# Kernel tuning notes

Hardware: AMD Instinct MI355X
Metric: run time of the kernel (lower is better)

The kernel has to match this reference:

```python
import jax, jax.numpy as jnp
import numpy as np

NUM_RELATIONS = 8
NUM_BASES = 4
IN_CH, HID, OUT_CH = 128, 64, 64
N_NODES, N_EDGES = 50000, 500000


def rgcn_conv(x, edge_src, edge_dst, edge_type, basis, comp, root, bias):
    """PyG RGCNConv with basis decomposition and per-relation mean aggregation.
    basis: [B, in, out], comp: [R, B], root: [in, out], bias: [out].
    W_r = sum_b comp[r, b] * basis[b]; msg_e = x[src_e] @ W_{type_e};
    aggregate mean over incoming edges per (node, relation), sum over relations,
    then add root transform and bias.
    """
    n = x.shape[0]
    out_dim = basis.shape[2]
    # Project once through all bases: [N, B, out]  (cheap: B=4)
    h = jnp.einsum('ni,bio->nbo', x, basis)
    # Per-edge message: contract gathered basis features with per-edge comp coeffs
    msg = jnp.einsum('eb,ebo->eo', comp[edge_type], h[edge_src])  # [E, out]
    # Mean aggregation per (dst, relation): segment id = dst*R + relation
    seg = edge_dst * NUM_RELATIONS + edge_type
    sums = jax.ops.segment_sum(msg, seg, num_segments=n * NUM_RELATIONS)
    cnt = jax.ops.segment_sum(jnp.ones((msg.shape[0], 1), msg.dtype), seg,
                              num_segments=n * NUM_RELATIONS)
    mean = sums / jnp.maximum(cnt, 1.0)
    agg = mean.reshape(n, NUM_RELATIONS, out_dim).sum(axis=1)
    return agg + x @ root + bias


def setup_inputs() -> dict:
    key = jax.random.key(0)
    ks = jax.random.split(key, 12)
    s1 = 1.0 / np.sqrt(IN_CH)
    s2 = 1.0 / np.sqrt(HID)
    return {
        'x': jax.random.normal(ks[0], (N_NODES, IN_CH), jnp.float32),
        'edge_index': jax.random.randint(ks[1], (2, N_EDGES), 0, N_NODES, jnp.int64),
        'edge_type': jax.random.randint(ks[2], (N_EDGES,), 0, NUM_RELATIONS, jnp.int64),
        'basis1': jax.random.normal(ks[3], (NUM_BASES, IN_CH, HID), jnp.float32) * s1,
        'comp1': jax.random.normal(ks[4], (NUM_RELATIONS, NUM_BASES), jnp.float32) * 0.5,
        'root1': jax.random.normal(ks[5], (IN_CH, HID), jnp.float32) * s1,
        'bias1': jnp.zeros((HID,), jnp.float32),
        'basis2': jax.random.normal(ks[6], (NUM_BASES, HID, OUT_CH), jnp.float32) * s2,
        'comp2': jax.random.normal(ks[7], (NUM_RELATIONS, NUM_BASES), jnp.float32) * 0.5,
        'root2': jax.random.normal(ks[8], (HID, OUT_CH), jnp.float32) * s2,
        'bias2': jnp.zeros((OUT_CH,), jnp.float32),
    }


def reference(x, edge_index, edge_type, basis1, comp1, root1, bias1,
              basis2, comp2, root2, bias2):
    src, dst = edge_index[0], edge_index[1]
    h = rgcn_conv(x, src, dst, edge_type, basis1, comp1, root1, bias1)
    h = jax.nn.relu(h)
    out = rgcn_conv(h, src, dst, edge_type, basis2, comp2, root2, bias2)
    return out
```

## Files before the change

kernel.cpp:

```cpp
#include <hip/hip_runtime.h>
#include <cstddef>

#define NREL 8
#define SCAN_TILE 4096

typedef __bf16 bf16x8 __attribute__((ext_vector_type(8)));
typedef float f32x4 __attribute__((ext_vector_type(4)));
typedef unsigned short ushort_t;

__device__ __forceinline__ unsigned f2bf_u(float f) {
    unsigned u = __float_as_uint(f);
    u += 0x7FFFu + ((u >> 16) & 1u);
    return u >> 16;
}
__device__ __forceinline__ short f2bf(float f) { return (short)f2bf_u(f); }
__device__ __forceinline__ int pack2bf(float lo, float hi) {
    return (int)(f2bf_u(lo) | (f2bf_u(hi) << 16));
}
__device__ __forceinline__ float bfval(unsigned short g) {
    return __uint_as_float((unsigned)g << 16);
}

__global__ __launch_bounds__(256) void zero_kernel(int4* __restrict__ p, int n16,
                                                   int* __restrict__ offsN, int E)
{
    int i = blockIdx.x * 256 + threadIdx.x;
    if (i < n16) p[i] = make_int4(0, 0, 0, 0);
    if (i == 0) *offsN = E;
}

template<int K>
__device__ __forceinline__ void wfrag_body(const float* __restrict__ basis,
                                           const float* __restrict__ root,
                                           const float* __restrict__ comp,
                                           short* __restrict__ Wf, int tid)
{
    constexpr int NK = K / 32;
    int lane = tid & 63, slot = tid >> 6;
    int ks = slot % NK, t = slot / NK;
    int kg = lane >> 4, lr = lane & 15;
    int k0 = ks * 32 + kg * 8;
    union { short s[8]; int4 v; } u;
#pragma unroll
    for (int e = 0; e < 8; ++e) {
        int k = k0 + e;
        float v;
        if (t < 32) {
            int rr = t >> 2, ch = (t & 3) * 16 + lr;
            v = comp[rr * 4 + 0] * basis[((size_t)0 * K + k) * 64 + ch]
              + comp[rr * 4 + 1] * basis[((size_t)1 * K + k) * 64 + ch]
              + comp[rr * 4 + 2] * basis[((size_t)2 * K + k) * 64 + ch]
              + comp[rr * 4 + 3] * basis[((size_t)3 * K + k) * 64 + ch];
        } else {
            v = root[(size_t)k * 64 + (t - 32) * 16 + lr];
        }
        u.s[e] = f2bf(v);
    }
    *(int4*)(Wf + (size_t)tid * 8) = u.v;
}

__device__ __forceinline__ void afrag_body128(const float* __restrict__ x,
                                              short* __restrict__ xf, int N, int tid)
{
    int lane = tid & 63, slot = tid >> 6;
    int ks = slot & 3, rt = slot >> 2;
    int kg = lane >> 4, lr = lane & 15;
    int row = rt * 16 + lr, k = ks * 32 + kg * 8;
    union { short s[8]; int4 v; } u;
    if (row < N) {
        const float* xp = x + (size_t)row * 128 + k;
        float4 a = *(const float4*)xp;
        float4 b = *(const float4*)(xp + 4);
        u.s[0] = f2bf(a.x); u.s[1] = f2bf(a.y); u.s[2] = f2bf(a.z); u.s[3] = f2bf(a.w);
        u.s[4] = f2bf(b.x); u.s[5] = f2bf(b.y); u.s[6] = f2bf(b.z); u.s[7] = f2bf(b.w);
    } else {
        u.v = make_int4(0, 0, 0, 0);
    }
    *(int4*)(xf + (size_t)tid * 8) = u.v;
}

__global__ __launch_bounds__(256) void prep_hist_kernel(
    const int* __restrict__ dstp, const int* __restrict__ et, int* __restrict__ cnt8,
    const float* __restrict__ basis1, const float* __restrict__ root1,
    const float* __restrict__ comp1,  const float* __restrict__ basis2,
    const float* __restrict__ root2,  const float* __restrict__ comp2,
    const float* __restrict__ x,
    short* __restrict__ Wf1, short* __restrict__ Wf2, short* __restrict__ xf1,
    int E, int N, int NT, int HB)
{
    int b = blockIdx.x;
    if (b < HB) {
        int e = b * 256 + threadIdx.x;
        if (e < E) atomicAdd(&cnt8[dstp[e] * NREL + et[e]], 1);
        return;
    }
    b -= HB;
    if (b < 36) { wfrag_body<128>(basis1, root1, comp1, Wf1, b * 256 + threadIdx.x); return; }
    b -= 36;
    if (b < 18) { wfrag_body<64>(basis2, root2, comp2, Wf2, b * 256 + threadIdx.x); return; }
    b -= 18;
    int tid = b * 256 + threadIdx.x;
    if (tid < NT * 256) afrag_body128(x, xf1, N, tid);
}

__global__ __launch_bounds__(256) void scan_part(const int* __restrict__ cnt8,
                                                 int* __restrict__ tsum, int n)
{
    int base = blockIdx.x * SCAN_TILE;
    int s = 0;
    for (int i = threadIdx.x; i < SCAN_TILE; i += 256) {
        int idx = base + i;
        if (idx < n) {
            int4 a = ((const int4*)cnt8)[idx * 2];
            int4 b = ((const int4*)cnt8)[idx * 2 + 1];
            s += a.x + a.y + a.z + a.w + b.x + b.y + b.z + b.w;
        }
    }
    for (int d = 1; d < 64; d <<= 1) s += __shfl_xor(s, d, 64);
    __shared__ int ws[4];
    if ((threadIdx.x & 63) == 0) ws[threadIdx.x >> 6] = s;
    __syncthreads();
    if (threadIdx.x == 0) tsum[blockIdx.x] = ws[0] + ws[1] + ws[2] + ws[3];
}

__global__ __launch_bounds__(256) void scan_final(const int* __restrict__ cnt8,
                                                  const int* __restrict__ tsum,
                                                  int* __restrict__ offs, int n)
{
    const int lane = threadIdx.x & 63, wid = threadIdx.x >> 6;
    int tbase = 0;
    for (int i = 0; i < blockIdx.x; ++i) tbase += tsum[i];
    int base = blockIdx.x * SCAN_TILE + threadIdx.x * 16;
    int v[16]; int s = 0;
#pragma unroll
    for (int j = 0; j < 16; ++j) {
        int idx = base + j;
        int dv = 0;
        if (idx < n) {
            int4 a = ((const int4*)cnt8)[idx * 2];
            int4 b = ((const int4*)cnt8)[idx * 2 + 1];
            dv = a.x + a.y + a.z + a.w + b.x + b.y + b.z + b.w;
        }
        v[j] = dv; s += dv;
    }
    int inc = s;
    for (int d = 1; d < 64; d <<= 1) {
        int t = __shfl_up(inc, d, 64);
        if (lane >= d) inc += t;
    }
    __shared__ int wsum[4];
    if (lane == 63) wsum[wid] = inc;
    __syncthreads();
    int run = tbase + (inc - s);
    for (int k = 0; k < wid; ++k) run += wsum[k];
#pragma unroll
    for (int j = 0; j < 16; ++j) {
        int idx = base + j;
        if (idx < n) offs[idx] = run;
        run += v[j];
    }
}

__global__ __launch_bounds__(256) void scatter_kernel(const int* __restrict__ src,
                                                      const int* __restrict__ dst,
                                                      const int* __restrict__ et,
                                                      const int* __restrict__ offs,
                                                      int* __restrict__ cursor,
                                                      const int* __restrict__ cnt8,
                                                      int4* __restrict__ edgeP, int E)
{
    int e = blockIdx.x * 256 + threadIdx.x;
    if (e >= E) return;
    int d = dst[e], r = et[e], s = src[e];
    int c = cnt8[d * NREL + r];
    float inv = 1.0f / (float)(c > 1 ? c : 1);
    int pos = offs[d] + atomicAdd(&cursor[d], 1);
    edgeP[pos] = make_int4((s * NREL + r) * 64, __float_as_int(inv), d, 0);
}

template<int K, bool L2OUT>
__global__ __launch_bounds__(256) void gemm_mfma(const short* __restrict__ xf,
                                                 const short* __restrict__ Wf,
                                                 const float* __restrict__ bias,
                                                 short* __restrict__ hr,
                                                 float* __restrict__ rootF,
                                                 int N, int gblk)
{
    constexpr int NK = K / 32;
    __shared__ short lds[4 * NK * 512];

    const int w = threadIdx.x >> 6, lane = threadIdx.x & 63;
    const int kg = lane >> 4, lr = lane & 15;
    const int g = blockIdx.y;

    {
        const int4* gsrc = (const int4*)(Wf + (size_t)g * 4 * NK * 512);
        int4* ldst = (int4*)lds;
        for (int i = threadIdx.x; i < 4 * NK * 64; i += 256)
            ldst[i] = gsrc[i];
    }

    float b0 = bias[lr], b1 = bias[16 + lr], b2 = bias[32 + lr], b3 = bias[48 + lr];

    __syncthreads();

    for (int bx = blockIdx.x; bx < gblk; bx += gridDim.x) {
        const int rt = bx * 4 + w;

        bf16x8 afrag[NK];
        const short* ap = xf + ((size_t)rt * NK * 64 + lane) * 8;
#pragma unroll
        for (int ks = 0; ks < NK; ++ks)
            afrag[ks] = *(const bf16x8*)(ap + ks * 512);

        f32x4 acc[4];
#pragma unroll
        for (int t = 0; t < 4; ++t) acc[t] = (f32x4){0.f, 0.f, 0.f, 0.f};

#pragma unroll
        for (int tt = 0; tt < 4; ++tt) {
#pragma unroll
            for (int ks = 0; ks < NK; ++ks) {
                bf16x8 bfrag = *(const bf16x8*)(lds + (tt * NK + ks) * 512 + lane * 8);
                acc[tt] = __builtin_amdgcn_mfma_f32_16x16x32_bf16(afrag[ks], bfrag,
                                                                  acc[tt], 0, 0, 0);
            }
        }

        const int drow0 = rt * 16 + kg * 4;
#pragma unroll
        for (int r = 0; r < 4; ++r) {
            int dr = drow0 + r;
            if (dr >= N) break;
            if (g < 8) {
                int u0 = pack2bf(acc[0][r], acc[1][r]);
                int u1 = pack2bf(acc[2][r], acc[3][r]);
                *(int2*)(hr + (size_t)dr * 512 + g * 64 + lr * 4) = make_int2(u0, u1);
            } else if (!L2OUT) {
                f32x4 o = {acc[0][r] + b0, acc[1][r] + b1, acc[2][r] + b2, acc[3][r] + b3};
                *(f32x4*)(rootF + (size_t)dr * 64 + lr * 4) = o;
            } else {
                rootF[(size_t)dr * 64 + lr]      = acc[0][r] + b0;
                rootF[(size_t)dr * 64 + 16 + lr] = acc[1][r] + b1;
                rootF[(size_t)dr * 64 + 32 + lr] = acc[2][r] + b2;
                rootF[(size_t)dr * 64 + 48 + lr] = acc[3][r] + b3;
            }
        }
    }
}

template<bool PERM>
__global__ __launch_bounds__(256) void agg_chunk_kernel(
    const int4* __restrict__ edgeP, const short* __restrict__ hr,
    float* __restrict__ accF, int E)
{
    const int w = threadIdx.x >> 6, l = threadIdx.x & 63;
    const int base = (blockIdx.x * 4 + w) * 32;
    if (base >= E) return;
    const int nv = min(32, E - base);

    int idx = base + (l & 31);
    if (idx >= E) idx = E - 1;
    int4 pl = edgeP[idx];

    const unsigned short* hp = (const unsigned short*)hr;

    int g[32];
#pragma unroll
    for (int j = 0; j < 32; ++j) {
        int hoff = __shfl(pl.x, j);
        g[j] = hp[(size_t)hoff + l];
    }

    const int co = PERM ? ((l & 3) * 16 + (l >> 2)) : l;

    float acc = 0.f;
#pragma unroll
    for (int j = 0; j < 32; ++j) {
        if (j >= nv) break;
        float invj = __uint_as_float(__shfl(pl.y, j));
        acc = fmaf(bfval((unsigned short)g[j]), invj, acc);
        int dcur = __shfl(pl.z, j);
        int dnxt = __shfl(pl.z, (j + 1) & 31);
        if (j == nv - 1 || dnxt != dcur) {
            unsafeAtomicAdd(&accF[(size_t)dcur * 64 + co], acc);
            acc = 0.f;
        }
    }
}

__global__ __launch_bounds__(256) void fin1_kernel(const float* __restrict__ aggF,
                                                   short* __restrict__ outB, int N)
{
    int i = blockIdx.x * 256 + threadIdx.x;
    if (i >= N * 64) return;
    int dst = i >> 6, l = i & 63;
    float v = fmaxf(aggF[i], 0.f);
    int tc = (l & 3) * 16 + (l >> 2);
    int rt2 = dst >> 4, lr2 = dst & 15;
    int ks2 = tc >> 5, kg2 = (tc >> 3) & 3, e2 = tc & 7;
    outB[(((size_t)rt2 * 2 + ks2) * 64 + kg2 * 16 + lr2) * 8 + e2] = f2bf(v);
}

extern "C" void kernel_launch(void* const* d_in, const int* in_sizes, int n_in,
                              void* d_out, int out_size, void* d_ws, size_t ws_size,
                              hipStream_t stream)
{
    const float* x      = (const float*)d_in[0];
    const int*   ei     = (const int*)d_in[1];
    const int*   et     = (const int*)d_in[2];
    const float* basis1 = (const float*)d_in[3];
    const float* comp1  = (const float*)d_in[4];
    const float* root1  = (const float*)d_in[5];
    const float* bias1  = (const float*)d_in[6];
    const float* basis2 = (const float*)d_in[7];
    const float* comp2  = (const float*)d_in[8];
    const float* root2  = (const float*)d_in[9];
    const float* bias2  = (const float*)d_in[10];
    float* out = (float*)d_out;

    const int N = in_sizes[0] / 128;
    const int E = in_sizes[2];
    const int* src  = ei;
    const int* dstp = ei + E;

    const int gblk = (N + 63) / 64;
    const int NT   = gblk * 4;
    const int HB   = (E + 255) / 256;

    char* p = (char*)d_ws;
    auto carve = [&](size_t bytes) -> char* {
        char* q = p; p += (bytes + 255) & ~(size_t)255; return q;
    };
    int*   cursor  = (int*)carve((size_t)N * 4);
    int*   cnt8    = (int*)carve((size_t)N * NREL * 4);
    char*  zend    = p;
    float* aggF1   = (float*)carve((size_t)N * 64 * 4);
    int*   offs    = (int*)carve((size_t)(N + 1) * 4);
    int*   tsum    = (int*)carve(256 * 4);
    int4*  edgeP   = (int4*)carve((size_t)E * 16);
    short* Wf1     = (short*)carve((size_t)36 * 4 * 64 * 8 * 2);
    short* Wf2     = (short*)carve((size_t)36 * 2 * 64 * 8 * 2);
    short* xf1     = (short*)carve((size_t)NT * 4 * 64 * 8 * 2);
    short* xf2     = (short*)carve((size_t)NT * 2 * 64 * 8 * 2);
    short* hr      = (short*)carve((size_t)N * 512 * 2);

    const int zn16 = (int)((zend - (char*)cursor) / 16);
    const int ntiles = (N + SCAN_TILE - 1) / SCAN_TILE;
    const int CHB = (E + 127) / 128;
    const int FB  = (N * 64 + 255) / 256;

    zero_kernel<<<(zn16 + 255) / 256, 256, 0, stream>>>((int4*)cursor, zn16, offs + N, E);

    prep_hist_kernel<<<HB + 36 + 18 + NT, 256, 0, stream>>>(
        dstp, et, cnt8, basis1, root1, comp1, basis2, root2, comp2, x,
        Wf1, Wf2, xf1, E, N, NT, HB);

    scan_part<<<ntiles, 256, 0, stream>>>(cnt8, tsum, N);
    scan_final<<<ntiles, 256, 0, stream>>>(cnt8, tsum, offs, N);

    scatter_kernel<<<HB, 256, 0, stream>>>(src, dstp, et, offs, cursor,
                                           cnt8, edgeP, E);

    gemm_mfma<128, false><<<dim3(256, 9), 256, 0, stream>>>(xf1, Wf1, bias1, hr,
                                                            aggF1, N, gblk);
    agg_chunk_kernel<false><<<CHB, 256, 0, stream>>>(edgeP, hr, aggF1, E);
    fin1_kernel<<<FB, 256, 0, stream>>>(aggF1, xf2, N);

    gemm_mfma<64, true><<<dim3(256, 9), 256, 0, stream>>>(xf2, Wf2, bias2, hr,
                                                          out, N, gblk);
    agg_chunk_kernel<true><<<CHB, 256, 0, stream>>>(edgeP, hr, out, E);
}
```

Measured before the change: 165.4 us.

## Process two edges per wavefront with 32-bit paired-channel gathers in aggregation

The aggregation kernel now gives each wavefront 64 edges, with half-waves handling even and odd edges. Each lane loads a 32-bit word holding two bf16 channels instead of one 16-bit value, and issues two atomics per flush. This halves the number of gather instructions and block launches, at the cost of twice as many atomics per lane and more complex validity and flush logic. The GEMM grid x-dimension also changes from a fixed 256 to half the block-group count, which alters how work is spread across blocks.

```diff
diff --git a/kernel.cpp b/kernel.cpp
--- a/kernel.cpp
+++ b/kernel.cpp
@@ -175,7 +175,7 @@
     int c = cnt8[d * NREL + r];
     float inv = 1.0f / (float)(c > 1 ? c : 1);
     int pos = offs[d] + atomicAdd(&cursor[d], 1);
-    edgeP[pos] = make_int4((s * NREL + r) * 64, __float_as_int(inv), d, 0);
+    edgeP[pos] = make_int4((s * NREL + r) * 32, __float_as_int(inv), d, 0);
 }
 
 template<int K, bool L2OUT>
@@ -255,36 +255,51 @@
     float* __restrict__ accF, int E)
 {
     const int w = threadIdx.x >> 6, l = threadIdx.x & 63;
-    const int base = (blockIdx.x * 4 + w) * 32;
+    const int half = l >> 5, c = l & 31;
+    const int base = (blockIdx.x * 4 + w) * 64;
     if (base >= E) return;
-    const int nv = min(32, E - base);
-
-    int idx = base + (l & 31);
+    const int nv = min(64, E - base);
+
+    int idx = base + 2 * c + half;
     if (idx >= E) idx = E - 1;
     int4 pl = edgeP[idx];
 
-    const unsigned short* hp = (const unsigned short*)hr;
-
-    int g[32];
+    const unsigned* hp32 = (const unsigned*)hr;
+
+    unsigned g[32];
 #pragma unroll
     for (int j = 0; j < 32; ++j) {
-        int hoff = __shfl(pl.x, j);
-        g[j] = hp[(size_t)hoff + l];
-    }
-
-    const int co = PERM ? ((l & 3) * 16 + (l >> 2)) : l;
-
-    float acc = 0.f;
+        int he = __shfl(pl.x, j);
+        int ho = __shfl(pl.x, 32 + j);
+        int hoff = half ? ho : he;
+        g[j] = hp32[(size_t)hoff + c];
+    }
+
+    int out0, out1;
+    if (PERM) {
+        int s0 = 2 * c, s1 = 2 * c + 1;
+        out0 = (s0 & 3) * 16 + (s0 >> 2);
+        out1 = (s1 & 3) * 16 + (s1 >> 2);
+    } else {
+        out0 = 2 * c; out1 = 2 * c + 1;
+    }
+
+    float a0 = 0.f, a1 = 0.f;
 #pragma unroll
     for (int j = 0; j < 32; ++j) {
-        if (j >= nv) break;
-        float invj = __uint_as_float(__shfl(pl.y, j));
-        acc = fmaf(bfval((unsigned short)g[j]), invj, acc);
-        int dcur = __shfl(pl.z, j);
-        int dnxt = __shfl(pl.z, (j + 1) & 31);
-        if (j == nv - 1 || dnxt != dcur) {
-            unsafeAtomicAdd(&accF[(size_t)dcur * 64 + co], acc);
-            acc = 0.f;
+        int jj = 2 * j + half;
+        bool valid = jj < nv;
+        float invj = __uint_as_float(__shfl(pl.y, half * 32 + j));
+        float v0 = bfval((unsigned short)(g[j] & 0xFFFFu));
+        float v1 = bfval((unsigned short)(g[j] >> 16));
+        if (valid) { a0 = fmaf(v0, invj, a0); a1 = fmaf(v1, invj, a1); }
+        int dcur = __shfl(pl.z, half * 32 + j);
+        int dnxt = (j < 31) ? __shfl(pl.z, half * 32 + j + 1) : -1;
+        bool flush = valid && (j == 31 || jj + 2 >= nv || dnxt != dcur);
+        if (flush) {
+            unsafeAtomicAdd(&accF[(size_t)dcur * 64 + out0], a0);
+            unsafeAtomicAdd(&accF[(size_t)dcur * 64 + out1], a1);
+            a0 = 0.f; a1 = 0.f;
         }
     }
 }
@@ -327,6 +342,7 @@
     const int gblk = (N + 63) / 64;
     const int NT   = gblk * 4;
     const int HB   = (E + 255) / 256;
+    const int GX   = (gblk + 1) / 2;
 
     char* p = (char*)d_ws;
     auto carve = [&](size_t bytes) -> char* {
@@ -347,7 +363,7 @@
 
     const int zn16 = (int)((zend - (char*)cursor) / 16);
     const int ntiles = (N + SCAN_TILE - 1) / SCAN_TILE;
-    const int CHB = (E + 127) / 128;
+    const int CHB = (E + 255) / 256;
     const int FB  = (N * 64 + 255) / 256;
 
     zero_kernel<<<(zn16 + 255) / 256, 256, 0, stream>>>((int4*)cursor, zn16, offs + N, E);
@@ -362,12 +378,12 @@
     scatter_kernel<<<HB, 256, 0, stream>>>(src, dstp, et, offs, cursor,
                                            cnt8, edgeP, E);
 
-    gemm_mfma<128, false><<<dim3(256, 9), 256, 0, stream>>>(xf1, Wf1, bias1, hr,
-                                                            aggF1, N, gblk);
+    gemm_mfma<128, false><<<dim3(GX, 9), 256, 0, stream>>>(xf1, Wf1, bias1, hr,
+                                                           aggF1, N, gblk);
     agg_chunk_kernel<false><<<CHB, 256, 0, stream>>>(edgeP, hr, aggF1, E);
     fin1_kernel<<<FB, 256, 0, stream>>>(aggF1, xf2, N);
 
-    gemm_mfma<64, true><<<dim3(256, 9), 256, 0, stream>>>(xf2, Wf2, bias2, hr,
-                                                          out, N, gblk);
+    gemm_mfma<64, true><<<dim3(GX, 9), 256, 0, stream>>>(xf2, Wf2, bias2, hr,
+                                                         out, N, gblk);
     agg_chunk_kernel<true><<<CHB, 256, 0, stream>>>(edgeP, hr, out, E);
 }
```

After: 249.9 us. 1.51x slower.
